# Performance work log

Measured on AMD Instinct MI355X. Metric: run time of the kernel, lower is better.

Reference implementation:

```python
import jax, jax.numpy as jnp
import numpy as np

IN_F = 2048
OUT_F = 2048
BATCH = 8192
ACT_BITS = 4
EPS = 1e-5


def setup_inputs() -> dict:
    key = jax.random.key(0)
    kx, kw, kb = jax.random.split(key, 3)
    x = jax.random.normal(kx, (BATCH, IN_F), dtype=jnp.float32)
    # kaiming-uniform-like init: bound = sqrt(6/fan_in) with a=sqrt(5) -> gain sqrt(2/(1+5))
    bound_w = float(np.sqrt(6.0 / (1.0 + 5.0)) / np.sqrt(IN_F))
    weight = jax.random.uniform(kw, (OUT_F, IN_F), minval=-bound_w, maxval=bound_w, dtype=jnp.float32)
    bound_b = float(1.0 / np.sqrt(IN_F))
    bias = jax.random.uniform(kb, (OUT_F,), minval=-bound_b, maxval=bound_b, dtype=jnp.float32)
    return {"x": x, "weight": weight, "bias": bias}


def _ste_sign(x):
    return x + jax.lax.stop_gradient(jnp.sign(x) - x)


def _ste_clip(x, lo, hi):
    return x + jax.lax.stop_gradient(jnp.clip(x, lo, hi) - x)


def reference(x, weight, bias):
    # weight binarization (ternary-ish via sign of mean-centered rows)
    w_centered = weight - jnp.mean(weight, axis=1, keepdims=True)
    w_bin = _ste_sign(w_centered)                       # [out, in]
    beta = jnp.mean(jnp.abs(weight), axis=1)[None, :]   # [1, out]
    # layer norm (no affine) over last dim
    mu = jnp.mean(x, axis=-1, keepdims=True)
    var = jnp.mean((x - mu) ** 2, axis=-1, keepdims=True)
    xln = (x - mu) / jnp.sqrt(var + EPS)
    qb = float(2 ** (ACT_BITS - 1) - 1)
    gama = jnp.maximum(jnp.max(jnp.abs(xln), axis=-1, keepdims=True), EPS)  # [B,1]
    xq = _ste_clip(xln * (qb / gama), -qb + EPS, qb - EPS)
    y = jnp.einsum('bi,oi->bo', xq, w_bin)
    y = y * (beta * gama / qb)
    return y + bias
```

## Files before the change

### kernel.cpp

```cpp
#include <hip/hip_runtime.h>
#include <hip/hip_bf16.h>

#define BATCH 8192
#define IN_F  2048
#define OUT_F 2048
#define QB    7.0f
#define EPSV  1e-5f
#define ASCALE 18.0f

typedef char  i8x4 __attribute__((ext_vector_type(4)));
typedef int   i32x4 __attribute__((ext_vector_type(4)));

#define AS1(p) ((__attribute__((address_space(1))) void*)(p))
#define AS3(p) ((__attribute__((address_space(3))) void*)(p))

__global__ __launch_bounds__(256) void prep_kernel(const float* __restrict__ x,
                                                   const float* __restrict__ w,
                                                   char* __restrict__ xq,
                                                   char* __restrict__ wb,
                                                   float* __restrict__ gamaOut,
                                                   float* __restrict__ betaOut) {
  const int t = threadIdx.x;
  const int wave = t >> 6, lane = t & 63;
  const int rowId = blockIdx.x * 4 + wave;

  if (rowId < OUT_F) {
    const int row = rowId;
    const float4* wr = (const float4*)(w + (size_t)row * IN_F);
    float4 v[8];
#pragma unroll
    for (int j = 0; j < 8; ++j) v[j] = wr[lane + 64 * j];

    float s = 0.0f, sa = 0.0f;
#pragma unroll
    for (int j = 0; j < 8; ++j) {
      s  += v[j].x + v[j].y + v[j].z + v[j].w;
      sa += fabsf(v[j].x) + fabsf(v[j].y) + fabsf(v[j].z) + fabsf(v[j].w);
    }
#pragma unroll
    for (int off = 32; off > 0; off >>= 1) {
      s  += __shfl_xor(s, off, 64);
      sa += __shfl_xor(sa, off, 64);
    }
    const float mu = s * (1.0f / IN_F);
    if (lane == 0) betaOut[row] = sa * (1.0f / IN_F);

    char* wbr = wb + (size_t)row * IN_F;
    auto sgn = [&](float xv) -> char {
      float d = xv - mu;
      return (char)((d > 0.0f) ? 1 : (d < 0.0f ? -1 : 0));
    };
#pragma unroll
    for (int j = 0; j < 8; ++j) {
      i8x4 q = { sgn(v[j].x), sgn(v[j].y), sgn(v[j].z), sgn(v[j].w) };
      ((i8x4*)wbr)[lane + 64 * j] = q;
    }
  } else {
    const int row = rowId - OUT_F;
    const float4* xr = (const float4*)(x + (size_t)row * IN_F);
    float4 v[8];
#pragma unroll
    for (int j = 0; j < 8; ++j) v[j] = xr[lane + 64 * j];

    float s = 0.0f, s2 = 0.0f;
#pragma unroll
    for (int j = 0; j < 8; ++j) {
      s  += v[j].x + v[j].y + v[j].z + v[j].w;
      s2 += v[j].x * v[j].x + v[j].y * v[j].y + v[j].z * v[j].z + v[j].w * v[j].w;
    }
#pragma unroll
    for (int off = 32; off > 0; off >>= 1) {
      s  += __shfl_xor(s, off, 64);
      s2 += __shfl_xor(s2, off, 64);
    }
    const float mu   = s * (1.0f / IN_F);
    const float rstd = rsqrtf(fmaxf(s2 * (1.0f / IN_F) - mu * mu, 0.0f) + EPSV);

    float ad = 0.0f;
#pragma unroll
    for (int j = 0; j < 8; ++j) {
      ad = fmaxf(ad, fmaxf(fmaxf(fabsf(v[j].x - mu), fabsf(v[j].y - mu)),
                           fmaxf(fabsf(v[j].z - mu), fabsf(v[j].w - mu))));
    }
#pragma unroll
    for (int off = 32; off > 0; off >>= 1) ad = fmaxf(ad, __shfl_xor(ad, off, 64));
    const float g = fmaxf(ad * rstd, EPSV);
    if (lane == 0) gamaOut[row] = g;

    const float c  = rstd * (QB * ASCALE) / g;
    const float lo = (-QB + EPSV) * ASCALE, hi = (QB - EPSV) * ASCALE;
    auto qz = [&](float vv) -> char {
      return (char)__float2int_rn(fminf(fmaxf((vv - mu) * c, lo), hi));
    };
    char* xqr = xq + (size_t)row * IN_F;
#pragma unroll
    for (int j = 0; j < 8; ++j) {
      i8x4 q = { qz(v[j].x), qz(v[j].y), qz(v[j].z), qz(v[j].w) };
      ((i8x4*)xqr)[lane + 64 * j] = q;
    }
  }
}

__global__ __launch_bounds__(256) void gemm_kernel(const char* __restrict__ A,
                                                   const char* __restrict__ B,
                                                   const float* __restrict__ beta,
                                                   const float* __restrict__ gama,
                                                   const float* __restrict__ bias,
                                                   float* __restrict__ out) {
  __shared__ __align__(16) char As[128 * 128];
  __shared__ __align__(16) char Bs[128 * 128];

  const int t = threadIdx.x;
  const int wave = t >> 6, lane = t & 63;
  const int mBase = blockIdx.y * 128;
  const int nBase = blockIdx.x * 128;
  const int wm = (wave >> 1) * 64;
  const int wn = (wave & 1) * 64;

  i32x4 acc[4][4];
#pragma unroll
  for (int i = 0; i < 4; ++i)
#pragma unroll
    for (int j = 0; j < 4; ++j) {
      i32x4 z = {0, 0, 0, 0};
      acc[i][j] = z;
    }

  const int lr = lane >> 3;
  const int ls = lane & 7;
  const int gch = (ls - lr) & 7;
  const char* aG[4];
  const char* bG[4];
  char* aL[4];
  char* bL[4];
#pragma unroll
  for (int j = 0; j < 4; ++j) {
    const int rowInTile = j * 32 + wave * 8 + lr;
    aG[j] = A + (size_t)(mBase + rowInTile) * IN_F + gch * 16;
    bG[j] = B + (size_t)(nBase + rowInTile) * IN_F + gch * 16;
    aL[j] = As + (j * 32 + wave * 8) * 128;
    bL[j] = Bs + (j * 32 + wave * 8) * 128;
  }

  const int fr = lane & 15;
  const int kq = lane >> 4;
  const char* aF = As + (wm + fr) * 128;
  const char* bF = Bs + (wn + fr) * 128;
  int koff[2];
#pragma unroll
  for (int ks = 0; ks < 2; ++ks) koff[ks] = ((ks * 4 + kq + fr) & 7) * 16;

  for (int k0 = 0; k0 < IN_F; k0 += 128) {
#pragma unroll
    for (int j = 0; j < 4; ++j) {
      __builtin_amdgcn_global_load_lds(AS1(aG[j] + k0), AS3(aL[j]), 16, 0, 0);
      __builtin_amdgcn_global_load_lds(AS1(bG[j] + k0), AS3(bL[j]), 16, 0, 0);
    }
    __syncthreads();

#pragma unroll
    for (int ks = 0; ks < 2; ++ks) {
      i32x4 af[4], bf[4];
#pragma unroll
      for (int mi = 0; mi < 4; ++mi) af[mi] = *(const i32x4*)(aF + mi * 16 * 128 + koff[ks]);
#pragma unroll
      for (int ni = 0; ni < 4; ++ni) bf[ni] = *(const i32x4*)(bF + ni * 16 * 128 + koff[ks]);
#pragma unroll
      for (int mi = 0; mi < 4; ++mi)
#pragma unroll
        for (int ni = 0; ni < 4; ++ni)
          acc[mi][ni] = __builtin_amdgcn_mfma_i32_16x16x64_i8(af[mi], bf[ni], acc[mi][ni], 0, 0, 0);
    }
    __syncthreads();
  }

  const float qinv = 1.0f / (QB * ASCALE);
  const int orow0 = mBase + wm + (kq << 2);
  const int ocol0 = nBase + wn + fr;
#pragma unroll
  for (int mi = 0; mi < 4; ++mi) {
    const int rbase = orow0 + mi * 16;
    const float g0 = gama[rbase + 0] * qinv;
    const float g1 = gama[rbase + 1] * qinv;
    const float g2 = gama[rbase + 2] * qinv;
    const float g3 = gama[rbase + 3] * qinv;
#pragma unroll
    for (int ni = 0; ni < 4; ++ni) {
      const int c = ocol0 + ni * 16;
      const float bsc = beta[c];
      const float bv  = bias[c];
      float* op = out + (size_t)rbase * OUT_F + c;
      op[0 * OUT_F] = (float)acc[mi][ni][0] * (bsc * g0) + bv;
      op[1 * OUT_F] = (float)acc[mi][ni][1] * (bsc * g1) + bv;
      op[2 * OUT_F] = (float)acc[mi][ni][2] * (bsc * g2) + bv;
      op[3 * OUT_F] = (float)acc[mi][ni][3] * (bsc * g3) + bv;
    }
  }
}

extern "C" void kernel_launch(void* const* d_in, const int* in_sizes, int n_in,
                              void* d_out, int out_size, void* d_ws, size_t ws_size,
                              hipStream_t stream) {
  const float* x      = (const float*)d_in[0];
  const float* weight = (const float*)d_in[1];
  const float* bias   = (const float*)d_in[2];
  float* out = (float*)d_out;

  char* ws = (char*)d_ws;
  char* wbin = ws;
  char* xq   = ws + (size_t)OUT_F * IN_F;
  float* betaW = (float*)(ws + (size_t)OUT_F * IN_F + (size_t)BATCH * IN_F);
  float* gamaX = betaW + OUT_F;

  prep_kernel<<<(OUT_F + BATCH) / 4, 256, 0, stream>>>(x, weight, xq, wbin, gamaX, betaW);
  gemm_kernel<<<dim3(OUT_F / 128, BATCH / 128), 256, 0, stream>>>(xq, wbin, betaW, gamaX, bias, out);
}
```

Measured before the change: 170.8 us.

## Double-buffer GEMM LDS tiles and swizzle block order across XCDs

```diff
diff --git a/kernel.cpp b/kernel.cpp
--- a/kernel.cpp
+++ b/kernel.cpp
@@ -107,13 +107,15 @@
                                                    const float* __restrict__ gama,
                                                    const float* __restrict__ bias,
                                                    float* __restrict__ out) {
-  __shared__ __align__(16) char As[128 * 128];
-  __shared__ __align__(16) char Bs[128 * 128];
+  __shared__ __align__(16) char As[2 * 128 * 128];
+  __shared__ __align__(16) char Bs[2 * 128 * 128];
 
   const int t = threadIdx.x;
   const int wave = t >> 6, lane = t & 63;
-  const int mBase = blockIdx.y * 128;
-  const int nBase = blockIdx.x * 128;
+  const int bid = blockIdx.x;
+  const int swz = (bid & 7) * 128 + (bid >> 3);
+  const int mBase = (swz >> 4) * 128;
+  const int nBase = (swz & 15) * 128;
   const int wm = (wave >> 1) * 64;
   const int wn = (wave & 1) * 64;
 
@@ -131,33 +133,31 @@
   const int gch = (ls - lr) & 7;
   const char* aG[4];
   const char* bG[4];
-  char* aL[4];
-  char* bL[4];
+  int lOff[4];
 #pragma unroll
   for (int j = 0; j < 4; ++j) {
     const int rowInTile = j * 32 + wave * 8 + lr;
     aG[j] = A + (size_t)(mBase + rowInTile) * IN_F + gch * 16;
     bG[j] = B + (size_t)(nBase + rowInTile) * IN_F + gch * 16;
-    aL[j] = As + (j * 32 + wave * 8) * 128;
-    bL[j] = Bs + (j * 32 + wave * 8) * 128;
+    lOff[j] = (j * 32 + wave * 8) * 128;
   }
 
   const int fr = lane & 15;
   const int kq = lane >> 4;
-  const char* aF = As + (wm + fr) * 128;
-  const char* bF = Bs + (wn + fr) * 128;
   int koff[2];
 #pragma unroll
   for (int ks = 0; ks < 2; ++ks) koff[ks] = ((ks * 4 + kq + fr) & 7) * 16;
 
-  for (int k0 = 0; k0 < IN_F; k0 += 128) {
+  auto stage = [&](int k0, int buf) {
 #pragma unroll
     for (int j = 0; j < 4; ++j) {
-      __builtin_amdgcn_global_load_lds(AS1(aG[j] + k0), AS3(aL[j]), 16, 0, 0);
-      __builtin_amdgcn_global_load_lds(AS1(bG[j] + k0), AS3(bL[j]), 16, 0, 0);
-    }
-    __syncthreads();
-
+      __builtin_amdgcn_global_load_lds(AS1(aG[j] + k0), AS3(As + buf * 16384 + lOff[j]), 16, 0, 0);
+      __builtin_amdgcn_global_load_lds(AS1(bG[j] + k0), AS3(Bs + buf * 16384 + lOff[j]), 16, 0, 0);
+    }
+  };
+  auto compute = [&](int buf) {
+    const char* aF = As + buf * 16384 + (wm + fr) * 128;
+    const char* bF = Bs + buf * 16384 + (wn + fr) * 128;
 #pragma unroll
     for (int ks = 0; ks < 2; ++ks) {
       i32x4 af[4], bf[4];
@@ -171,8 +171,19 @@
         for (int ni = 0; ni < 4; ++ni)
           acc[mi][ni] = __builtin_amdgcn_mfma_i32_16x16x64_i8(af[mi], bf[ni], acc[mi][ni], 0, 0, 0);
     }
+  };
+
+  stage(0, 0);
+  __syncthreads();
+
+  int cur = 0;
+  for (int k0 = 128; k0 < IN_F; k0 += 128) {
+    stage(k0, cur ^ 1);
+    compute(cur);
     __syncthreads();
-  }
+    cur ^= 1;
+  }
+  compute(cur);
 
   const float qinv = 1.0f / (QB * ASCALE);
   const int orow0 = mBase + wm + (kq << 2);
@@ -213,5 +224,5 @@
   float* gamaX = betaW + OUT_F;
 
   prep_kernel<<<(OUT_F + BATCH) / 4, 256, 0, stream>>>(x, weight, xq, wbin, gamaX, betaW);
-  gemm_kernel<<<dim3(OUT_F / 128, BATCH / 128), 256, 0, stream>>>(xq, wbin, betaW, gamaX, bias, out);
+  gemm_kernel<<<OUT_F / 128 * (BATCH / 128), 256, 0, stream>>>(xq, wbin, betaW, gamaX, bias, out);
 }
```

Result: faster. 166.8 us (-2.3%).
